# Kernel tuning notes

Hardware: AMD Instinct MI355X
Metric: run time of the kernel (lower is better)

The kernel has to match this reference:

```python
import jax, jax.numpy as jnp
import numpy as np

B, S, H, D = 4, 2048, 16, 64


def setup_inputs() -> dict:
    key = jax.random.key(0)
    kq, kk, kv, kl = jax.random.split(key, 4)
    qs = jax.random.normal(kq, (B, S, H, D), dtype=jnp.float32)
    ks = jax.random.normal(kk, (B, S, H, D), dtype=jnp.float32)
    vs = jax.random.normal(kv, (B, S, H, D), dtype=jnp.float32)
    # valid lengths in [S//2, S] so no sequence is fully masked out
    valid_lens = jax.random.randint(kl, (B,), S // 2, S + 1, dtype=jnp.int32)
    return {"qs": qs, "ks": ks, "vs": vs, "valid_lens": valid_lens}


def reference(qs, ks, vs, valid_lens):
    # ScanAttention == exact softmax attention (FlashAttention-2 is an
    # IO-aware reformulation of the same math). qs scaled by 1/sqrt(D).
    d = qs.shape[-1]
    scale = 1.0 / jnp.sqrt(jnp.asarray(d, qs.dtype))
    # scores: [B, H, Q, K]
    scores = jnp.einsum('bqhd,bkhd->bhqk', qs * scale, ks)
    # key mask from valid_lens: position k is valid iff k < valid_lens[b]
    k_len = ks.shape[1]
    ks_mask = jnp.arange(k_len)[None, :] < valid_lens[:, None]  # [B, K]
    scores = jnp.where(ks_mask[:, None, None, :], scores, -jnp.inf)
    attn = jax.nn.softmax(scores, axis=-1)
    ctx = jnp.einsum('bhqk,bkhd->bqhd', attn, vs)
    return ctx
```

## Files before the change

kernel.cpp:

```cpp
#include <hip/hip_runtime.h>
#include <hip/hip_bf16.h>

typedef __bf16 bf16x8 __attribute__((ext_vector_type(8)));
typedef float  f32x4  __attribute__((ext_vector_type(4)));
typedef float  f32x16 __attribute__((ext_vector_type(16)));
typedef float  f4     __attribute__((ext_vector_type(4)));
typedef unsigned int u32;
typedef u32 u32x4 __attribute__((ext_vector_type(4)));

#define MFMA16(a,b,c) __builtin_amdgcn_mfma_f32_16x16x32_bf16(a,b,c,0,0,0)
#define MFMA32(a,b,c) __builtin_amdgcn_mfma_f32_32x32x16_bf16(a,b,c,0,0,0)

constexpr int   Bc = 4, Sc = 2048, Hc = 16, Dc = 64;
constexpr int   HD  = Hc * Dc;
constexpr int   SHD = Sc * HD;
constexpr float SCALE = 0.125f;
constexpr float LOG2E = 1.4426950408889634f;
constexpr float QSC   = SCALE * LOG2E;
constexpr float NEG   = -1e30f;
constexpr int   HEAD_ELEMS = Sc * Dc;
constexpr size_t KV_ELEMS  = (size_t)Bc * Hc * HEAD_ELEMS;

__global__ __launch_bounds__(256) void prep2(
    const float* __restrict__ K, const float* __restrict__ V,
    __bf16* __restrict__ Kf, __bf16* __restrict__ Vf)
{
    __shared__ __align__(16) __bf16 KT[64][80];
    __shared__ __align__(16) __bf16 VT[64][80];

    const int bid = blockIdx.x;
    const int st  = bid & 31;
    const int h   = (bid >> 5) & 15;
    const int b   = bid >> 9;
    const int tid = threadIdx.x;
    const int sl  = tid >> 2;
    const int d0  = (tid & 3) * 16;
    const size_t iof = ((size_t)(b * 2048 + st * 64 + sl) * 16 + h) * 64 + d0;

    #pragma unroll
    for (int q = 0; q < 2; ++q) {
        f4 a = __builtin_nontemporal_load((const f4*)(K + iof + q * 8));
        f4 c = __builtin_nontemporal_load((const f4*)(K + iof + q * 8 + 4));
        bf16x8 w;
        w[0]=(__bf16)a.x; w[1]=(__bf16)a.y; w[2]=(__bf16)a.z; w[3]=(__bf16)a.w;
        w[4]=(__bf16)c.x; w[5]=(__bf16)c.y; w[6]=(__bf16)c.z; w[7]=(__bf16)c.w;
        *(bf16x8*)&KT[sl][d0 + q * 8] = w;
    }
    #pragma unroll
    for (int q = 0; q < 2; ++q) {
        f4 a = __builtin_nontemporal_load((const f4*)(V + iof + q * 8));
        f4 c = __builtin_nontemporal_load((const f4*)(V + iof + q * 8 + 4));
        bf16x8 w;
        w[0]=(__bf16)a.x; w[1]=(__bf16)a.y; w[2]=(__bf16)a.z; w[3]=(__bf16)a.w;
        w[4]=(__bf16)c.x; w[5]=(__bf16)c.y; w[6]=(__bf16)c.z; w[7]=(__bf16)c.w;
        *(bf16x8*)&VT[sl][d0 + q * 8] = w;
    }
    __syncthreads();

    const size_t hbase = (size_t)(b * 16 + h) * HEAD_ELEMS;

    #pragma unroll
    for (int it = 0; it < 2; ++it) {
        const int idx = it * 256 + tid;
        const int tl  = idx >> 8;
        const int dk  = (idx >> 6) & 3;
        const int ln  = idx & 63;
        const int l31 = ln & 31, lhi = ln >> 5;
        bf16x8 w = *(const bf16x8*)&KT[tl * 32 + l31][dk * 16 + lhi * 8];
        *(bf16x8*)(Kf + hbase + (size_t)(((st * 2 + tl) * 4 + dk) * 512 + ln * 8)) = w;
    }
    #pragma unroll
    for (int it = 0; it < 2; ++it) {
        const int idx  = it * 256 + tid;
        const int tl   = idx >> 8;
        const int dblk = (idx >> 7) & 1;
        const int kt2  = (idx >> 6) & 1;
        const int ln   = idx & 63;
        const int l31  = ln & 31, lhi = ln >> 5;
        bf16x8 w;
        #pragma unroll
        for (int j = 0; j < 8; ++j)
            w[j] = VT[tl * 32 + kt2 * 16 + lhi * 8 + j][dblk * 32 + l31];
        *(bf16x8*)(Vf + hbase +
            (size_t)(((((st * 2 + tl) * 2 + dblk) * 2 + kt2)) * 512 + ln * 8)) = w;
    }
}

__global__ __launch_bounds__(256, 4) void fattn4(
    const float* __restrict__ Q, const __bf16* __restrict__ Kf,
    const __bf16* __restrict__ Vf, const int* __restrict__ VL,
    float* __restrict__ O)
{
    const int bid  = blockIdx.x;
    const int h    = (bid & 7) + 8 * ((bid >> 3) & 1);
    const int qt   = bid >> 4;
    const int w    = threadIdx.x >> 6;
    const int b    = (w + (qt >> 4)) & 3;
    const int head = b * 16 + h;
    const int lane = threadIdx.x & 63;
    const int l31  = lane & 31;
    const int hi   = lane >> 5;
    const int vl   = VL[b];

    const size_t qbase = (size_t)b * SHD + (size_t)h * Dc;
    const __bf16* kfh = Kf + (size_t)head * HEAD_ELEMS + lane * 8;
    const __bf16* vfh = Vf + (size_t)head * HEAD_ELEMS + lane * 8;
    const int qrow0 = qt * 32;

    bf16x8 qf[4];
    {
        const float* qp = Q + qbase + (size_t)(qrow0 + l31) * HD + hi * 8;
        #pragma unroll
        for (int dk = 0; dk < 4; ++dk) {
            f4 x0 = __builtin_nontemporal_load((const f4*)(qp + dk * 16));
            f4 x1 = __builtin_nontemporal_load((const f4*)(qp + dk * 16 + 4));
            bf16x8 f;
            f[0]=(__bf16)(x0.x*QSC); f[1]=(__bf16)(x0.y*QSC);
            f[2]=(__bf16)(x0.z*QSC); f[3]=(__bf16)(x0.w*QSC);
            f[4]=(__bf16)(x1.x*QSC); f[5]=(__bf16)(x1.y*QSC);
            f[6]=(__bf16)(x1.z*QSC); f[7]=(__bf16)(x1.w*QSC);
            qf[dk] = f;
        }
    }

    f32x16 acc0, acc1;
    #pragma unroll
    for (int i = 0; i < 16; ++i) { acc0[i] = 0.f; acc1[i] = 0.f; }
    float m = NEG, lsum = 0.f;

    const int nt   = (vl + 31) >> 5;
    const int ntm1 = nt - 1;
    const bool hastail = (vl & 31) != 0;

    bf16x8 kf[4], vf[4];
    #pragma unroll
    for (int dk = 0; dk < 4; ++dk) kf[dk] = *(const bf16x8*)(kfh + dk * 512);
    #pragma unroll
    for (int i = 0; i < 4; ++i)   vf[i]  = *(const bf16x8*)(vfh + i * 512);

    for (int t = 0; t < nt; ++t) {
        f32x16 s;
        #pragma unroll
        for (int i = 0; i < 16; ++i) s[i] = 0.f;
        #pragma unroll
        for (int dk = 0; dk < 4; ++dk) s = MFMA32(kf[dk], qf[dk], s);

        {
            const size_t off = (size_t)((t < ntm1) ? t + 1 : t) * 2048;
            #pragma unroll
            for (int dk = 0; dk < 4; ++dk)
                kf[dk] = *(const bf16x8*)(kfh + off + dk * 512);
        }

        if (t == ntm1 && hastail) {
            const int kv0 = t * 32;
            #pragma unroll
            for (int i = 0; i < 16; ++i) {
                const int key = kv0 + (i & 3) + 8 * (i >> 2) + 4 * hi;
                if (key >= vl) s[i] = NEG;
            }
        }

        float c0 = fmaxf(fmaxf(s[0],  s[1]),  s[2]);
        float c1 = fmaxf(fmaxf(s[3],  s[4]),  s[5]);
        float c2 = fmaxf(fmaxf(s[6],  s[7]),  s[8]);
        float c3 = fmaxf(fmaxf(s[9],  s[10]), s[11]);
        float c4 = fmaxf(fmaxf(s[12], s[13]), s[14]);
        float c5 = fmaxf(fmaxf(c0, c1), s[15]);
        float c6 = fmaxf(fmaxf(c2, c3), c4);
        float tm = fmaxf(c5, c6);
        tm = fmaxf(tm, __shfl_xor(tm, 32));

        if (__any(tm > m + 8.0f)) {
            const float mn  = fmaxf(m, tm);
            const float fac = __builtin_amdgcn_exp2f(m - mn);
            lsum *= fac;
            #pragma unroll
            for (int i = 0; i < 16; ++i) { acc0[i] *= fac; acc1[i] *= fac; }
            m = mn;
        }
        #pragma unroll
        for (int i = 0; i < 16; ++i)
            s[i] = __builtin_amdgcn_exp2f(s[i] - m);
        {
            float t0 = (s[0]+s[1]) + (s[2]+s[3]);
            float t1 = (s[4]+s[5]) + (s[6]+s[7]);
            float t2 = (s[8]+s[9]) + (s[10]+s[11]);
            float t3 = (s[12]+s[13]) + (s[14]+s[15]);
            lsum += (t0 + t1) + (t2 + t3);
        }

        bf16x8 ap[2];
        #pragma unroll
        for (int kt = 0; kt < 2; ++kt) {
            u32 w0, w1, w2, w3;
            asm("v_cvt_pk_bf16_f32 %0, %1, %2" : "=v"(w0) : "v"(s[8*kt+0]), "v"(s[8*kt+1]));
            asm("v_cvt_pk_bf16_f32 %0, %1, %2" : "=v"(w1) : "v"(s[8*kt+2]), "v"(s[8*kt+3]));
            asm("v_cvt_pk_bf16_f32 %0, %1, %2" : "=v"(w2) : "v"(s[8*kt+4]), "v"(s[8*kt+5]));
            asm("v_cvt_pk_bf16_f32 %0, %1, %2" : "=v"(w3) : "v"(s[8*kt+6]), "v"(s[8*kt+7]));
            asm("v_permlane32_swap_b32 %0, %1" : "+v"(w0), "+v"(w2));
            asm("v_permlane32_swap_b32 %0, %1" : "+v"(w1), "+v"(w3));
            u32x4 fw;
            fw.x = w0;
            fw.y = w1;
            fw.z = w2;
            fw.w = w3;
            ap[kt] = __builtin_bit_cast(bf16x8, fw);
        }

        acc0 = MFMA32(vf[0], ap[0], acc0);
        acc0 = MFMA32(vf[1], ap[1], acc0);
        acc1 = MFMA32(vf[2], ap[0], acc1);
        acc1 = MFMA32(vf[3], ap[1], acc1);

        {
            const size_t off = (size_t)((t < ntm1) ? t + 1 : t) * 2048;
            #pragma unroll
            for (int i = 0; i < 4; ++i)
                vf[i] = *(const bf16x8*)(vfh + off + i * 512);
        }
    }

    const float lfull = lsum + __shfl_xor(lsum, 32);
    const float linv  = 1.0f / lfull;
    float* op = O + qbase + (size_t)(qrow0 + l31) * HD;
    #pragma unroll
    for (int qd = 0; qd < 4; ++qd) {
        f4 w0, w1;
        w0.x = acc0[4*qd+0]*linv; w0.y = acc0[4*qd+1]*linv;
        w0.z = acc0[4*qd+2]*linv; w0.w = acc0[4*qd+3]*linv;
        w1.x = acc1[4*qd+0]*linv; w1.y = acc1[4*qd+1]*linv;
        w1.z = acc1[4*qd+2]*linv; w1.w = acc1[4*qd+3]*linv;
        *(f4*)(op + qd * 8 + 4 * hi)      = w0;
        *(f4*)(op + 32 + qd * 8 + 4 * hi) = w1;
    }
}

__global__ __launch_bounds__(256, 2) void fattn_fb(
    const float* __restrict__ Q, const float* __restrict__ K,
    const float* __restrict__ V, const int* __restrict__ VL,
    float* __restrict__ O)
{
    __shared__ __bf16 Vts[64 * 64];
    __shared__ __bf16 Pl[4][32 * 64];
    const int bid = blockIdx.x;
    const int qt = bid & 15, h = (bid >> 4) & 15, b = bid >> 8;
    const int tid = threadIdx.x, wid = tid >> 6, lane = tid & 63;
    const int li = lane & 15, lg = lane >> 4;
    const int vl = VL[b];
    const size_t base = (size_t)b * SHD + (size_t)h * Dc;
    bf16x8 aq[2][2];
    const int qrow0 = qt * 128 + wid * 32;
    #pragma unroll
    for (int m = 0; m < 2; ++m) {
        const float* qp = Q + base + (size_t)(qrow0 + m * 16 + li) * HD + lg * 8;
        #pragma unroll
        for (int ks = 0; ks < 2; ++ks) {
            float4 x0 = *(const float4*)(qp + ks * 32);
            float4 x1 = *(const float4*)(qp + ks * 32 + 4);
            bf16x8 f;
            f[0]=(__bf16)(x0.x*QSC); f[1]=(__bf16)(x0.y*QSC);
            f[2]=(__bf16)(x0.z*QSC); f[3]=(__bf16)(x0.w*QSC);
            f[4]=(__bf16)(x1.x*QSC); f[5]=(__bf16)(x1.y*QSC);
            f[6]=(__bf16)(x1.z*QSC); f[7]=(__bf16)(x1.w*QSC);
            aq[m][ks] = f;
        }
    }
    bf16x8 bones;
    #pragma unroll
    for (int j = 0; j < 8; ++j) bones[j] = (__bf16)1.0f;
    f32x4 acc[2][4]; float mst[2][4], lst[2][4];
    #pragma unroll
    for (int m = 0; m < 2; ++m) {
        #pragma unroll
        for (int r = 0; r < 4; ++r) { mst[m][r] = NEG; lst[m][r] = 0.f; }
        #pragma unroll
        for (int dt = 0; dt < 4; ++dt)
            #pragma unroll
            for (int r = 0; r < 4; ++r) acc[m][dt][r] = 0.f;
    }
    const int ntiles = (vl + 63) >> 6;
    const int sd = tid & 63, skb = (tid >> 6) * 8;
    const float* vpd = V + base + sd;
    for (int t = 0; t < ntiles; ++t) {
        const int kv0 = t * 64;
        __syncthreads();
        #pragma unroll
        for (int rep = 0; rep < 2; ++rep) {
            const int kb2 = skb + rep * 32;
            bf16x8 pk;
            #pragma unroll
            for (int j = 0; j < 8; ++j) pk[j] = (__bf16)vpd[(size_t)(kv0+kb2+j)*HD];
            *(bf16x8*)&Vts[(sd*64+kb2) ^ ((sd&7)<<3)] = pk;
        }
        __syncthreads();
        f32x4 s[2][4];
        #pragma unroll
        for (int m = 0; m < 2; ++m)
            #pragma unroll
            for (int nt2 = 0; nt2 < 4; ++nt2)
                #pragma unroll
                for (int r = 0; r < 4; ++r) s[m][nt2][r] = 0.f;
        #pragma unroll
        for (int nt2 = 0; nt2 < 4; ++nt2) {
            const float* kp = K + base + (size_t)(kv0+nt2*16+li)*HD + lg*8;
            #pragma unroll
            for (int ks = 0; ks < 2; ++ks) {
                float4 x0 = *(const float4*)(kp + ks*32);
                float4 x1 = *(const float4*)(kp + ks*32 + 4);
                bf16x8 f;
                f[0]=(__bf16)x0.x; f[1]=(__bf16)x0.y; f[2]=(__bf16)x0.z; f[3]=(__bf16)x0.w;
                f[4]=(__bf16)x1.x; f[5]=(__bf16)x1.y; f[6]=(__bf16)x1.z; f[7]=(__bf16)x1.w;
                #pragma unroll
                for (int m = 0; m < 2; ++m) s[m][nt2] = MFMA16(aq[m][ks], f, s[m][nt2]);
            }
        }
        bool kva[4];
        #pragma unroll
        for (int nt2 = 0; nt2 < 4; ++nt2) kva[nt2] = (kv0 + nt2*16 + li) < vl;
        #pragma unroll
        for (int m = 0; m < 2; ++m)
            #pragma unroll
            for (int nt2 = 0; nt2 < 4; ++nt2)
                #pragma unroll
                for (int r = 0; r < 4; ++r)
                    if (!kva[nt2]) s[m][nt2][r] = NEG;
        #pragma unroll
        for (int m = 0; m < 2; ++m) {
            #pragma unroll
            for (int r = 0; r < 4; ++r) {
                float tmx = fmaxf(fmaxf(s[m][0][r], s[m][1][r]),
                                  fmaxf(s[m][2][r], s[m][3][r]));
                tmx = fmaxf(tmx, __shfl_xor(tmx, 1));
                tmx = fmaxf(tmx, __shfl_xor(tmx, 2));
                tmx = fmaxf(tmx, __shfl_xor(tmx, 4));
                tmx = fmaxf(tmx, __shfl_xor(tmx, 8));
                const float mn = fmaxf(mst[m][r], tmx);
                const float fac = __builtin_amdgcn_exp2f(mst[m][r] - mn);
                mst[m][r] = mn; lst[m][r] *= fac;
                #pragma unroll
                for (int dt = 0; dt < 4; ++dt) acc[m][dt][r] *= fac;
                const int qr = m*16 + lg*4 + r, swz = (qr & 7) << 3;
                #pragma unroll
                for (int nt2 = 0; nt2 < 4; ++nt2)
                    Pl[wid][(qr*64 + nt2*16 + li) ^ swz] =
                        (__bf16)__builtin_amdgcn_exp2f(s[m][nt2][r] - mn);
            }
        }
        bf16x8 ap[2][2];
        #pragma unroll
        for (int m = 0; m < 2; ++m) {
            const int qr = m*16 + li, swz = (qr & 7) << 3;
            #pragma unroll
            for (int ks = 0; ks < 2; ++ks)
                ap[m][ks] = *(bf16x8*)&Pl[wid][(qr*64 + ks*32 + lg*8) ^ swz];
        }
        #pragma unroll
        for (int m = 0; m < 2; ++m) {
            f32x4 rs;
            #pragma unroll
            for (int r = 0; r < 4; ++r) rs[r] = 0.f;
            rs = MFMA16(ap[m][0], bones, rs);
            rs = MFMA16(ap[m][1], bones, rs);
            #pragma unroll
            for (int r = 0; r < 4; ++r) lst[m][r] += rs[r];
        }
        #pragma unroll
        for (int dt = 0; dt < 4; ++dt) {
            const int d = dt*16 + li, swz = (d & 7) << 3;
            #pragma unroll
            for (int ks = 0; ks < 2; ++ks) {
                bf16x8 bv = *(bf16x8*)&Vts[(d*64 + ks*32 + lg*8) ^ swz];
                #pragma unroll
                for (int m = 0; m < 2; ++m)
                    acc[m][dt] = MFMA16(ap[m][ks], bv, acc[m][dt]);
            }
        }
    }
    #pragma unroll
    for (int m = 0; m < 2; ++m) {
        #pragma unroll
        for (int r = 0; r < 4; ++r) {
            const float inv = 1.0f / lst[m][r];
            float* op = O + base + (size_t)(qrow0 + m*16 + lg*4 + r) * HD;
            #pragma unroll
            for (int dt = 0; dt < 4; ++dt) op[dt*16 + li] = acc[m][dt][r] * inv;
        }
    }
}

extern "C" void kernel_launch(void* const* d_in, const int* in_sizes, int n_in,
                              void* d_out, int out_size, void* d_ws, size_t ws_size,
                              hipStream_t stream) {
    (void)in_sizes; (void)n_in; (void)out_size;
    const float* q    = (const float*)d_in[0];
    const float* k    = (const float*)d_in[1];
    const float* v    = (const float*)d_in[2];
    const int*   vlen = (const int*)d_in[3];
    float*       out  = (float*)d_out;
    const size_t need = 2 * KV_ELEMS * sizeof(__bf16);
    if (ws_size >= need) {
        __bf16* kfp = (__bf16*)d_ws;
        __bf16* vfp = kfp + KV_ELEMS;
        prep2<<<dim3(2048), 256, 0, stream>>>(k, v, kfp, vfp);
        fattn4<<<dim3(1024), 256, 0, stream>>>(q, kfp, vfp, vlen, out);
    } else {
        fattn_fb<<<dim3(1024), 256, 0, stream>>>(q, k, v, vlen, out);
    }
}
```

Measured before the change: 120.7 us.

## Split KV range across wave pairs and merge partial softmax via LDS

Each block now pairs two waves per 32-row query tile. Each wave processes half of the key tiles, and the two partial (m, l, acc) states are merged through shared memory before the output is written. The grid doubles to 2048 blocks and the occupancy hint rises to 6. The register prefetch of the next K/V tile is dropped in favour of in-loop loads. This shortens the serial per-wave KV loop and raises parallelism, at the cost of LDS traffic, a block barrier, and losing the software prefetch.

```diff
diff --git a/kernel.cpp b/kernel.cpp
--- a/kernel.cpp
+++ b/kernel.cpp
@@ -86,21 +86,28 @@
     }
 }
 
-__global__ __launch_bounds__(256, 4) void fattn4(
+__global__ __launch_bounds__(256, 6) void fattn5(
     const float* __restrict__ Q, const __bf16* __restrict__ Kf,
     const __bf16* __restrict__ Vf, const int* __restrict__ VL,
     float* __restrict__ O)
 {
-    const int bid  = blockIdx.x;
-    const int h    = (bid & 7) + 8 * ((bid >> 3) & 1);
-    const int qt   = bid >> 4;
-    const int w    = threadIdx.x >> 6;
-    const int b    = (w + (qt >> 4)) & 3;
-    const int head = b * 16 + h;
-    const int lane = threadIdx.x & 63;
-    const int l31  = lane & 31;
-    const int hi   = lane >> 5;
-    const int vl   = VL[b];
+    __shared__ float Lacc[2][32][65];
+    __shared__ float Lml[2][32][2];
+
+    const int bid   = blockIdx.x;
+    const int h     = (bid & 7) + 8 * ((bid >> 3) & 1);
+    const int qpair = (bid >> 4) & 31;
+    const int z     = bid >> 9;
+    const int b     = (z + qpair) & 3;
+    const int w     = threadIdx.x >> 6;
+    const int qt    = qpair * 2 + (w >> 1);
+    const int half  = w & 1;
+    const int slot  = w >> 1;
+    const int head  = b * 16 + h;
+    const int lane  = threadIdx.x & 63;
+    const int l31   = lane & 31;
+    const int hi    = lane >> 5;
+    const int vl    = VL[b];
 
     const size_t qbase = (size_t)b * SHD + (size_t)h * Dc;
     const __bf16* kfh = Kf + (size_t)head * HEAD_ELEMS + lane * 8;
@@ -128,31 +135,29 @@
     for (int i = 0; i < 16; ++i) { acc0[i] = 0.f; acc1[i] = 0.f; }
     float m = NEG, lsum = 0.f;
 
-    const int nt   = (vl + 31) >> 5;
-    const int ntm1 = nt - 1;
+    const int ntot = (vl + 31) >> 5;
+    const int nh0  = (ntot + 1) >> 1;
+    const int t0   = half ? nh0 : 0;
+    const int t1   = half ? ntot : nh0;
     const bool hastail = (vl & 31) != 0;
 
-    bf16x8 kf[4], vf[4];
-    #pragma unroll
-    for (int dk = 0; dk < 4; ++dk) kf[dk] = *(const bf16x8*)(kfh + dk * 512);
-    #pragma unroll
-    for (int i = 0; i < 4; ++i)   vf[i]  = *(const bf16x8*)(vfh + i * 512);
-
-    for (int t = 0; t < nt; ++t) {
+    for (int t = t0; t < t1; ++t) {
+        const size_t off = (size_t)t * 2048;
+
+        bf16x8 kf0 = *(const bf16x8*)(kfh + off);
+        bf16x8 kf1 = *(const bf16x8*)(kfh + off + 512);
+        bf16x8 kf2 = *(const bf16x8*)(kfh + off + 1024);
+        bf16x8 kf3 = *(const bf16x8*)(kfh + off + 1536);
+
         f32x16 s;
         #pragma unroll
         for (int i = 0; i < 16; ++i) s[i] = 0.f;
-        #pragma unroll
-        for (int dk = 0; dk < 4; ++dk) s = MFMA32(kf[dk], qf[dk], s);
-
-        {
-            const size_t off = (size_t)((t < ntm1) ? t + 1 : t) * 2048;
-            #pragma unroll
-            for (int dk = 0; dk < 4; ++dk)
-                kf[dk] = *(const bf16x8*)(kfh + off + dk * 512);
-        }
-
-        if (t == ntm1 && hastail) {
+        s = MFMA32(kf0, qf[0], s);
+        s = MFMA32(kf1, qf[1], s);
+        s = MFMA32(kf2, qf[2], s);
+        s = MFMA32(kf3, qf[3], s);
+
+        if (t == ntot - 1 && hastail) {
             const int kv0 = t * 32;
             #pragma unroll
             for (int i = 0; i < 16; ++i) {
@@ -183,11 +188,11 @@
         for (int i = 0; i < 16; ++i)
             s[i] = __builtin_amdgcn_exp2f(s[i] - m);
         {
-            float t0 = (s[0]+s[1]) + (s[2]+s[3]);
-            float t1 = (s[4]+s[5]) + (s[6]+s[7]);
-            float t2 = (s[8]+s[9]) + (s[10]+s[11]);
-            float t3 = (s[12]+s[13]) + (s[14]+s[15]);
-            lsum += (t0 + t1) + (t2 + t3);
+            float u0 = (s[0]+s[1]) + (s[2]+s[3]);
+            float u1 = (s[4]+s[5]) + (s[6]+s[7]);
+            float u2 = (s[8]+s[9]) + (s[10]+s[11]);
+            float u3 = (s[12]+s[13]) + (s[14]+s[15]);
+            lsum += (u0 + u1) + (u2 + u3);
         }
 
         bf16x8 ap[2];
@@ -201,38 +206,71 @@
             asm("v_permlane32_swap_b32 %0, %1" : "+v"(w0), "+v"(w2));
             asm("v_permlane32_swap_b32 %0, %1" : "+v"(w1), "+v"(w3));
             u32x4 fw;
-            fw.x = w0;
-            fw.y = w1;
-            fw.z = w2;
-            fw.w = w3;
+            fw.x = w0; fw.y = w1; fw.z = w2; fw.w = w3;
             ap[kt] = __builtin_bit_cast(bf16x8, fw);
         }
 
-        acc0 = MFMA32(vf[0], ap[0], acc0);
-        acc0 = MFMA32(vf[1], ap[1], acc0);
-        acc1 = MFMA32(vf[2], ap[0], acc1);
-        acc1 = MFMA32(vf[3], ap[1], acc1);
-
-        {
-            const size_t off = (size_t)((t < ntm1) ? t + 1 : t) * 2048;
-            #pragma unroll
-            for (int i = 0; i < 4; ++i)
-                vf[i] = *(const bf16x8*)(vfh + off + i * 512);
-        }
+        bf16x8 vf0 = *(const bf16x8*)(vfh + off);
+        bf16x8 vf1 = *(const bf16x8*)(vfh + off + 512);
+        bf16x8 vf2 = *(const bf16x8*)(vfh + off + 1024);
+        bf16x8 vf3 = *(const bf16x8*)(vfh + off + 1536);
+        acc0 = MFMA32(vf0, ap[0], acc0);
+        acc0 = MFMA32(vf1, ap[1], acc0);
+        acc1 = MFMA32(vf2, ap[0], acc1);
+        acc1 = MFMA32(vf3, ap[1], acc1);
     }
 
     const float lfull = lsum + __shfl_xor(lsum, 32);
-    const float linv  = 1.0f / lfull;
-    float* op = O + qbase + (size_t)(qrow0 + l31) * HD;
-    #pragma unroll
-    for (int qd = 0; qd < 4; ++qd) {
-        f4 w0, w1;
-        w0.x = acc0[4*qd+0]*linv; w0.y = acc0[4*qd+1]*linv;
-        w0.z = acc0[4*qd+2]*linv; w0.w = acc0[4*qd+3]*linv;
-        w1.x = acc1[4*qd+0]*linv; w1.y = acc1[4*qd+1]*linv;
-        w1.z = acc1[4*qd+2]*linv; w1.w = acc1[4*qd+3]*linv;
-        *(f4*)(op + qd * 8 + 4 * hi)      = w0;
-        *(f4*)(op + 32 + qd * 8 + 4 * hi) = w1;
+
+    if (half) {
+        #pragma unroll
+        for (int dt = 0; dt < 2; ++dt) {
+            #pragma unroll
+            for (int qd = 0; qd < 4; ++qd) {
+                f4 v;
+                if (dt == 0) {
+                    v.x = acc0[4*qd+0]; v.y = acc0[4*qd+1];
+                    v.z = acc0[4*qd+2]; v.w = acc0[4*qd+3];
+                } else {
+                    v.x = acc1[4*qd+0]; v.y = acc1[4*qd+1];
+                    v.z = acc1[4*qd+2]; v.w = acc1[4*qd+3];
+                }
+                *(f4*)&Lacc[slot][l31][dt*32 + qd*8 + 4*hi] = v;
+            }
+        }
+        Lml[slot][l31][0] = m;
+        Lml[slot][l31][1] = lfull;
+    }
+    __syncthreads();
+    if (!half) {
+        const float mB = Lml[slot][l31][0];
+        const float lB = Lml[slot][l31][1];
+        const float M  = fmaxf(m, mB);
+        const float fA = __builtin_amdgcn_exp2f(m - M);
+        const float fB = __builtin_amdgcn_exp2f(mB - M);
+        const float linv = 1.0f / (lfull * fA + lB * fB);
+        const float cA = fA * linv, cB = fB * linv;
+        float* op = O + qbase + (size_t)(qrow0 + l31) * HD;
+        #pragma unroll
+        for (int dt = 0; dt < 2; ++dt) {
+            #pragma unroll
+            for (int qd = 0; qd < 4; ++qd) {
+                f4 vB = *(const f4*)&Lacc[slot][l31][dt*32 + qd*8 + 4*hi];
+                f4 o;
+                if (dt == 0) {
+                    o.x = acc0[4*qd+0]*cA + vB.x*cB;
+                    o.y = acc0[4*qd+1]*cA + vB.y*cB;
+                    o.z = acc0[4*qd+2]*cA + vB.z*cB;
+                    o.w = acc0[4*qd+3]*cA + vB.w*cB;
+                } else {
+                    o.x = acc1[4*qd+0]*cA + vB.x*cB;
+                    o.y = acc1[4*qd+1]*cA + vB.y*cB;
+                    o.z = acc1[4*qd+2]*cA + vB.z*cB;
+                    o.w = acc1[4*qd+3]*cA + vB.w*cB;
+                }
+                *(f4*)(op + dt * 32 + qd * 8 + 4 * hi) = o;
+            }
+        }
     }
 }
 
@@ -403,7 +441,7 @@
         __bf16* kfp = (__bf16*)d_ws;
         __bf16* vfp = kfp + KV_ELEMS;
         prep2<<<dim3(2048), 256, 0, stream>>>(k, v, kfp, vfp);
-        fattn4<<<dim3(1024), 256, 0, stream>>>(q, kfp, vfp, vlen, out);
+        fattn5<<<dim3(2048), 256, 0, stream>>>(q, kfp, vfp, vlen, out);
     } else {
         fattn_fb<<<dim3(1024), 256, 0, stream>>>(q, k, v, vlen, out);
     }
```

Result: slower. 188.1 us (+55.8%).
